# Kernel tuning notes

Measured on AMD Instinct MI355X. Metric: run time of the kernel, lower is better.

The kernel has to match this reference:

```python
import jax, jax.numpy as jnp
import numpy as np

TEMPERATURE = 0.07
NUM_NEGATIVES = 128
B, C, H, W = 4, 256, 32, 32
N_TOTAL = B * H * W  # 4096


def setup_inputs() -> dict:
    key = jax.random.key(0)
    k1, k2, k3 = jax.random.split(key, 3)
    feat_q = jax.random.normal(k1, (B, C, H, W), dtype=jnp.float32)
    feat_k = jax.random.normal(k2, (B, C, H, W), dtype=jnp.float32)
    # uniform draws in [0, N_TOTAL-1): same distribution as indexing into the
    # length-(N-1) 'choices' array in the original per-i loop
    neg_indices = jax.random.randint(k3, (N_TOTAL, NUM_NEGATIVES), 0, N_TOTAL - 1, dtype=jnp.int64 if jax.config.jax_enable_x64 else jnp.int32)
    return {"feat_q": feat_q, "feat_k": feat_k, "neg_indices": neg_indices}


def reference(feat_q, feat_k, neg_indices):
    b, c, h, w = feat_q.shape
    n = b * h * w
    q = feat_q.reshape(b, c, -1)
    k = feat_k.reshape(b, c, -1)
    # F.normalize(dim=1), eps=1e-12
    q = q / jnp.maximum(jnp.linalg.norm(q, axis=1, keepdims=True), 1e-12)
    k = k / jnp.maximum(jnp.linalg.norm(k, axis=1, keepdims=True), 1e-12)
    q = q.transpose(0, 2, 1).reshape(-1, c)  # [N, C]
    k = k.transpose(0, 2, 1).reshape(-1, c)  # [N, C]
    l_pos = jnp.sum(q * k, axis=1, keepdims=True)  # [N, 1]
    # self-exclusion: choices = all_idx without i -> shift sampled idx >= i up by 1
    row = jnp.arange(n, dtype=neg_indices.dtype)[:, None]
    idx = neg_indices + (neg_indices >= row).astype(neg_indices.dtype)  # [N, K]
    k_neg = k[idx]  # [N, K, C] gather
    l_neg = jnp.einsum('nc,nkc->nk', q, k_neg)  # [N, K]
    logits = jnp.concatenate([l_pos, l_neg], axis=1) / TEMPERATURE  # [N, 1+K]
    # cross-entropy with label 0 for every row
    loss = jnp.mean(jax.nn.logsumexp(logits, axis=1) - logits[:, 0])
    return loss
```

## Files before the change

### kernel.cpp

```cpp
#include <hip/hip_runtime.h>
#include <hip/hip_bf16.h>

#define N_TOTAL 4096
#define C_DIM 256
#define K_NEG 128
#define HW 1024
#define TEMP_INV (1.0f / 0.07f)

typedef _Float16 h8 __attribute__((ext_vector_type(8)));

__global__ __launch_bounds__(256) void ss_kernel(
    const float* __restrict__ fq, const float* __restrict__ fk,
    float* __restrict__ ss) {
  const int bid = blockIdx.x;
  const int tensor = bid >> 8;
  const int sp = (bid >> 2) & 63;
  const int cc = bid & 3;
  const float* in = tensor ? fk : fq;
  const int n0 = sp * 64;
  const int b = n0 / HW, s0 = n0 % HW;
  const float* base = in + (size_t)b * C_DIM * HW + s0;

  const int t = threadIdx.x, lane = t & 63, w = t >> 6;
  float acc = 0.f;
#pragma unroll
  for (int i = 0; i < 16; ++i) {
    float v = base[(size_t)(cc * 64 + w * 16 + i) * HW + lane];
    acc = fmaf(v, v, acc);
  }
  __shared__ float red[4][64];
  red[w][lane] = acc;
  __syncthreads();
  if (w == 0) {
    float tot = red[0][lane] + red[1][lane] + red[2][lane] + red[3][lane];
    atomicAdd(&ss[tensor * N_TOTAL + n0 + lane], tot);
  }
}

__global__ __launch_bounds__(256) void tr_kernel(
    const float* __restrict__ fq, const float* __restrict__ fk,
    const float* __restrict__ ss,
    _Float16* __restrict__ qh, _Float16* __restrict__ kh) {
  const int bid = blockIdx.x;
  const int tensor = bid >> 8;
  const int sp = (bid >> 2) & 63;
  const int cc = bid & 3;
  const float* in = tensor ? fk : fq;
  _Float16* out = tensor ? kh : qh;
  const int n0 = sp * 64;
  const int b = n0 / HW, s0 = n0 % HW;
  const float* base = in + (size_t)b * C_DIM * HW + s0;

  const int t = threadIdx.x, lane = t & 63, w = t >> 6;

  __shared__ float tile[64][65];
  __shared__ float sinv[64];
  if (w == 0) {
    float ssv = ss[tensor * N_TOTAL + n0 + lane];
    sinv[lane] = 1.0f / fmaxf(sqrtf(ssv), 1e-12f);
  }
#pragma unroll
  for (int i = 0; i < 16; ++i) {
    int cl = w * 16 + i;
    tile[cl][lane] = base[(size_t)(cc * 64 + cl) * HW + lane];
  }
  __syncthreads();
#pragma unroll
  for (int i = 0; i < 16; ++i) {
    int row = w * 16 + i;
    out[(size_t)(n0 + row) * C_DIM + cc * 64 + lane] =
        (_Float16)(tile[lane][row] * sinv[row]);
  }
}

__global__ __launch_bounds__(256) void nce_kernel(
    const _Float16* __restrict__ qh, const _Float16* __restrict__ kh,
    const int* __restrict__ neg, float* __restrict__ loss_buf) {
  const int n = blockIdx.x;
  const int t = threadIdx.x;
  const int lane = t & 63;
  const int w = t >> 6;
  const int sub = lane & 7;
  const int unit = w * 8 + (lane >> 3);

  __shared__ float sneg[K_NEG];
  __shared__ float s_lpos;

  int r[4];
#pragma unroll
  for (int j = 0; j < 4; ++j) {
    int x = neg[(size_t)n * K_NEG + j * 32 + unit];
    r[j] = x + (x >= n ? 1 : 0);
  }
  const h8* qrow = (const h8*)(qh + (size_t)n * C_DIM) + sub * 4;
  h8 qv[4];
#pragma unroll
  for (int i = 0; i < 4; ++i) qv[i] = qrow[i];
  h8 kd[4][4];
#pragma unroll
  for (int j = 0; j < 4; ++j) {
    const h8* kr = (const h8*)(kh + (size_t)r[j] * C_DIM) + sub * 4;
#pragma unroll
    for (int i = 0; i < 4; ++i) kd[j][i] = kr[i];
  }
  h8 kp[4];
  if (unit == 0) {
    const h8* kr = (const h8*)(kh + (size_t)n * C_DIM) + sub * 4;
#pragma unroll
    for (int i = 0; i < 4; ++i) kp[i] = kr[i];
  }

  float qf[32];
#pragma unroll
  for (int i = 0; i < 4; ++i)
#pragma unroll
    for (int j = 0; j < 8; ++j) qf[i * 8 + j] = (float)qv[i][j];

#pragma unroll
  for (int j = 0; j < 4; ++j) {
    float a0 = 0.f, a1 = 0.f;
#pragma unroll
    for (int i = 0; i < 4; ++i) {
#pragma unroll
      for (int e = 0; e < 8; e += 2) {
        a0 = fmaf((float)kd[j][i][e], qf[i * 8 + e], a0);
        a1 = fmaf((float)kd[j][i][e + 1], qf[i * 8 + e + 1], a1);
      }
    }
    float acc = a0 + a1;
    acc += __shfl_xor(acc, 1);
    acc += __shfl_xor(acc, 2);
    acc += __shfl_xor(acc, 4);
    if (sub == 0) sneg[j * 32 + unit] = acc;
  }
  if (unit == 0) {
    float a0 = 0.f, a1 = 0.f;
#pragma unroll
    for (int i = 0; i < 4; ++i) {
#pragma unroll
      for (int e = 0; e < 8; e += 2) {
        a0 = fmaf((float)kp[i][e], qf[i * 8 + e], a0);
        a1 = fmaf((float)kp[i][e + 1], qf[i * 8 + e + 1], a1);
      }
    }
    float acc = a0 + a1;
    acc += __shfl_xor(acc, 1);
    acc += __shfl_xor(acc, 2);
    acc += __shfl_xor(acc, 4);
    if (sub == 0) s_lpos = acc;
  }
  __syncthreads();

  if (w == 0) {
    float lp = s_lpos * TEMP_INV;
    float x1 = sneg[lane] * TEMP_INV;
    float x2 = sneg[lane + 64] * TEMP_INV;
    float m = fmaxf(fmaxf(x1, x2), lp);
#pragma unroll
    for (int off = 32; off; off >>= 1) m = fmaxf(m, __shfl_xor(m, off));
    float s = __expf(x1 - m) + __expf(x2 - m);
#pragma unroll
    for (int off = 32; off; off >>= 1) s += __shfl_xor(s, off);
    if (lane == 0) loss_buf[n] = m + __logf(s) - lp;
  }
}

__global__ __launch_bounds__(1024) void reduce_kernel(
    const float* __restrict__ loss_buf, float* __restrict__ out) {
  const int t = threadIdx.x;
  const float4 v = ((const float4*)loss_buf)[t];
  float s = (v.x + v.y) + (v.z + v.w);
#pragma unroll
  for (int off = 32; off; off >>= 1) s += __shfl_xor(s, off);
  __shared__ float red[16];
  if ((t & 63) == 0) red[t >> 6] = s;
  __syncthreads();
  if (t < 16) {
    float x = red[t];
#pragma unroll
    for (int off = 8; off; off >>= 1) x += __shfl_xor(x, off);
    if (t == 0) out[0] = x * (1.0f / N_TOTAL);
  }
}

extern "C" void kernel_launch(void* const* d_in, const int* in_sizes, int n_in,
                              void* d_out, int out_size, void* d_ws,
                              size_t ws_size, hipStream_t stream) {
  const float* fq = (const float*)d_in[0];
  const float* fk = (const float*)d_in[1];
  const int* neg = (const int*)d_in[2];
  float* out = (float*)d_out;

  _Float16* qh = (_Float16*)d_ws;
  _Float16* kh = qh + (size_t)N_TOTAL * C_DIM;
  float* ss = (float*)(kh + (size_t)N_TOTAL * C_DIM);
  float* loss_buf = ss + 2 * N_TOTAL;

  hipMemsetAsync(ss, 0, 2 * N_TOTAL * sizeof(float), stream);
  hipLaunchKernelGGL(ss_kernel, dim3(512), dim3(256), 0, stream, fq, fk, ss);
  hipLaunchKernelGGL(tr_kernel, dim3(512), dim3(256), 0, stream,
                     fq, fk, ss, qh, kh);
  hipLaunchKernelGGL(nce_kernel, dim3(N_TOTAL), dim3(256), 0, stream,
                     qh, kh, neg, loss_buf);
  hipLaunchKernelGGL(reduce_kernel, dim3(1), dim3(1024), 0, stream,
                     loss_buf, out);
}
```

Baseline: 93.06 us.

## Fuse norm and transpose kernels, defer normalization into NCE dot products

Merges the sum-of-squares and transpose/cast kernels into one pass that reads each input tile once. The fp16 tiles are stored unnormalized, and each dot product is scaled by the inverse norms inside the NCE kernel, which removes a kernel launch and a second full read of the inputs. It also vectorizes the global loads (float4) and stores (8-wide fp16), and changes the per-lane k-row access to an interleaved pattern for better coalescing. In exchange the NCE kernel does extra scattered loads of norms, and storing unnormalized values in fp16 could lose precision if magnitudes are large.

```diff
diff --git a/kernel.cpp b/kernel.cpp
--- a/kernel.cpp
+++ b/kernel.cpp
@@ -9,38 +9,10 @@
 
 typedef _Float16 h8 __attribute__((ext_vector_type(8)));
 
-__global__ __launch_bounds__(256) void ss_kernel(
+__global__ __launch_bounds__(256) void tr_ss_kernel(
     const float* __restrict__ fq, const float* __restrict__ fk,
+    _Float16* __restrict__ qh, _Float16* __restrict__ kh,
     float* __restrict__ ss) {
-  const int bid = blockIdx.x;
-  const int tensor = bid >> 8;
-  const int sp = (bid >> 2) & 63;
-  const int cc = bid & 3;
-  const float* in = tensor ? fk : fq;
-  const int n0 = sp * 64;
-  const int b = n0 / HW, s0 = n0 % HW;
-  const float* base = in + (size_t)b * C_DIM * HW + s0;
-
-  const int t = threadIdx.x, lane = t & 63, w = t >> 6;
-  float acc = 0.f;
-#pragma unroll
-  for (int i = 0; i < 16; ++i) {
-    float v = base[(size_t)(cc * 64 + w * 16 + i) * HW + lane];
-    acc = fmaf(v, v, acc);
-  }
-  __shared__ float red[4][64];
-  red[w][lane] = acc;
-  __syncthreads();
-  if (w == 0) {
-    float tot = red[0][lane] + red[1][lane] + red[2][lane] + red[3][lane];
-    atomicAdd(&ss[tensor * N_TOTAL + n0 + lane], tot);
-  }
-}
-
-__global__ __launch_bounds__(256) void tr_kernel(
-    const float* __restrict__ fq, const float* __restrict__ fk,
-    const float* __restrict__ ss,
-    _Float16* __restrict__ qh, _Float16* __restrict__ kh) {
   const int bid = blockIdx.x;
   const int tensor = bid >> 8;
   const int sp = (bid >> 2) & 63;
@@ -52,30 +24,49 @@
   const float* base = in + (size_t)b * C_DIM * HW + s0;
 
   const int t = threadIdx.x, lane = t & 63, w = t >> 6;
-
   __shared__ float tile[64][65];
-  __shared__ float sinv[64];
+  __shared__ float red[4][64];
+
+  const int chl = t >> 4;
+  const int sp4 = (t & 15) * 4;
+#pragma unroll
+  for (int p = 0; p < 4; ++p) {
+    int cl = p * 16 + chl;
+    const float4 v =
+        *(const float4*)(base + (size_t)(cc * 64 + cl) * HW + sp4);
+    tile[cl][sp4] = v.x; tile[cl][sp4 + 1] = v.y;
+    tile[cl][sp4 + 2] = v.z; tile[cl][sp4 + 3] = v.w;
+  }
+  __syncthreads();
+
+  float acc = 0.f;
+#pragma unroll
+  for (int j = 0; j < 16; ++j) {
+    float v = tile[w * 16 + j][lane];
+    acc = fmaf(v, v, acc);
+  }
+  red[w][lane] = acc;
+  __syncthreads();
   if (w == 0) {
-    float ssv = ss[tensor * N_TOTAL + n0 + lane];
-    sinv[lane] = 1.0f / fmaxf(sqrtf(ssv), 1e-12f);
-  }
-#pragma unroll
-  for (int i = 0; i < 16; ++i) {
-    int cl = w * 16 + i;
-    tile[cl][lane] = base[(size_t)(cc * 64 + cl) * HW + lane];
-  }
-  __syncthreads();
-#pragma unroll
-  for (int i = 0; i < 16; ++i) {
-    int row = w * 16 + i;
-    out[(size_t)(n0 + row) * C_DIM + cc * 64 + lane] =
-        (_Float16)(tile[lane][row] * sinv[row]);
-  }
+    float tot = red[0][lane] + red[1][lane] + red[2][lane] + red[3][lane];
+    atomicAdd(&ss[tensor * N_TOTAL + n0 + lane], tot);
+  }
+
+  const int wsp = t >> 2, q4 = t & 3;
+  h8 o0, o1;
+#pragma unroll
+  for (int j = 0; j < 8; ++j) o0[j] = (_Float16)tile[q4 * 16 + j][wsp];
+#pragma unroll
+  for (int j = 0; j < 8; ++j) o1[j] = (_Float16)tile[q4 * 16 + 8 + j][wsp];
+  h8* dst = (h8*)(out + (size_t)(n0 + wsp) * C_DIM + cc * 64 + q4 * 16);
+  dst[0] = o0;
+  dst[1] = o1;
 }
 
 __global__ __launch_bounds__(256) void nce_kernel(
     const _Float16* __restrict__ qh, const _Float16* __restrict__ kh,
-    const int* __restrict__ neg, float* __restrict__ loss_buf) {
+    const float* __restrict__ ss, const int* __restrict__ neg,
+    float* __restrict__ loss_buf) {
   const int n = blockIdx.x;
   const int t = threadIdx.x;
   const int lane = t & 63;
@@ -86,68 +77,82 @@
   __shared__ float sneg[K_NEG];
   __shared__ float s_lpos;
 
+  const float* ssk_arr = ss + N_TOTAL;
+
   int r[4];
 #pragma unroll
   for (int j = 0; j < 4; ++j) {
     int x = neg[(size_t)n * K_NEG + j * 32 + unit];
     r[j] = x + (x >= n ? 1 : 0);
   }
-  const h8* qrow = (const h8*)(qh + (size_t)n * C_DIM) + sub * 4;
+  const h8* qrow = (const h8*)(qh + (size_t)n * C_DIM);
   h8 qv[4];
 #pragma unroll
-  for (int i = 0; i < 4; ++i) qv[i] = qrow[i];
+  for (int i = 0; i < 4; ++i) qv[i] = qrow[i * 8 + sub];
   h8 kd[4][4];
 #pragma unroll
   for (int j = 0; j < 4; ++j) {
-    const h8* kr = (const h8*)(kh + (size_t)r[j] * C_DIM) + sub * 4;
-#pragma unroll
-    for (int i = 0; i < 4; ++i) kd[j][i] = kr[i];
-  }
+    const h8* kr = (const h8*)(kh + (size_t)r[j] * C_DIM);
+#pragma unroll
+    for (int i = 0; i < 4; ++i) kd[j][i] = kr[i * 8 + sub];
+  }
+  float ssk[4];
+#pragma unroll
+  for (int j = 0; j < 4; ++j) ssk[j] = ssk_arr[r[j]];
+  float ssq = ss[n];
   h8 kp[4];
+  float sskp = 1.f;
   if (unit == 0) {
-    const h8* kr = (const h8*)(kh + (size_t)n * C_DIM) + sub * 4;
-#pragma unroll
-    for (int i = 0; i < 4; ++i) kp[i] = kr[i];
+    const h8* kr = (const h8*)(kh + (size_t)n * C_DIM);
+#pragma unroll
+    for (int i = 0; i < 4; ++i) kp[i] = kr[i * 8 + sub];
+    sskp = ssk_arr[n];
   }
 
   float qf[32];
 #pragma unroll
   for (int i = 0; i < 4; ++i)
 #pragma unroll
-    for (int j = 0; j < 8; ++j) qf[i * 8 + j] = (float)qv[i][j];
+    for (int e = 0; e < 8; ++e) qf[i * 8 + e] = (float)qv[i][e];
+
+  const float invq = 1.0f / fmaxf(sqrtf(ssq), 1e-12f);
 
 #pragma unroll
   for (int j = 0; j < 4; ++j) {
     float a0 = 0.f, a1 = 0.f;
 #pragma unroll
-    for (int i = 0; i < 4; ++i) {
+    for (int i = 0; i < 4; ++i)
 #pragma unroll
       for (int e = 0; e < 8; e += 2) {
         a0 = fmaf((float)kd[j][i][e], qf[i * 8 + e], a0);
         a1 = fmaf((float)kd[j][i][e + 1], qf[i * 8 + e + 1], a1);
       }
-    }
     float acc = a0 + a1;
     acc += __shfl_xor(acc, 1);
     acc += __shfl_xor(acc, 2);
     acc += __shfl_xor(acc, 4);
-    if (sub == 0) sneg[j * 32 + unit] = acc;
+    if (sub == 0) {
+      float invk = 1.0f / fmaxf(sqrtf(ssk[j]), 1e-12f);
+      sneg[j * 32 + unit] = acc * invq * invk;
+    }
   }
   if (unit == 0) {
     float a0 = 0.f, a1 = 0.f;
 #pragma unroll
-    for (int i = 0; i < 4; ++i) {
+    for (int i = 0; i < 4; ++i)
 #pragma unroll
       for (int e = 0; e < 8; e += 2) {
         a0 = fmaf((float)kp[i][e], qf[i * 8 + e], a0);
         a1 = fmaf((float)kp[i][e + 1], qf[i * 8 + e + 1], a1);
       }
-    }
     float acc = a0 + a1;
     acc += __shfl_xor(acc, 1);
     acc += __shfl_xor(acc, 2);
     acc += __shfl_xor(acc, 4);
-    if (sub == 0) s_lpos = acc;
+    if (sub == 0) {
+      float invk = 1.0f / fmaxf(sqrtf(sskp), 1e-12f);
+      s_lpos = acc * invq * invk;
+    }
   }
   __syncthreads();
 
@@ -197,11 +202,10 @@
   float* loss_buf = ss + 2 * N_TOTAL;
 
   hipMemsetAsync(ss, 0, 2 * N_TOTAL * sizeof(float), stream);
-  hipLaunchKernelGGL(ss_kernel, dim3(512), dim3(256), 0, stream, fq, fk, ss);
-  hipLaunchKernelGGL(tr_kernel, dim3(512), dim3(256), 0, stream,
-                     fq, fk, ss, qh, kh);
+  hipLaunchKernelGGL(tr_ss_kernel, dim3(512), dim3(256), 0, stream,
+                     fq, fk, qh, kh, ss);
   hipLaunchKernelGGL(nce_kernel, dim3(N_TOTAL), dim3(256), 0, stream,
-                     qh, kh, neg, loss_buf);
+                     qh, kh, ss, neg, loss_buf);
   hipLaunchKernelGGL(reduce_kernel, dim3(1), dim3(1024), 0, stream,
                      loss_buf, out);
 }
```

Measured after the change: 89.63 us. 1.04x faster.
